# Kernel optimization log

Hardware: AMD Instinct MI355X
Metric: run time of the kernel (lower is better)

The kernel has to match this reference:

```python
import jax, jax.numpy as jnp
import numpy as np

B, S, D = 4, 2048, 1024
NEG = 1e9


def setup_inputs() -> dict:
    key = jax.random.key(0)
    ks = jax.random.split(key, 4)
    scale = 1.0 / np.sqrt(D)  # glorot-ish init scale for stability
    x = jax.random.normal(ks[0], (B, S, D), dtype=jnp.float32)
    Wq = jax.random.normal(ks[1], (D, D), dtype=jnp.float32) * scale
    Wk = jax.random.normal(ks[2], (D, D), dtype=jnp.float32) * scale
    Wv = jax.random.normal(ks[3], (D, D), dtype=jnp.float32) * scale
    bq = jnp.zeros((D,), jnp.float32)
    bk = jnp.zeros((D,), jnp.float32)
    bv = jnp.zeros((D,), jnp.float32)
    return {"x": x, "Wq": Wq, "bq": bq, "Wk": Wk, "bk": bk, "Wv": Wv, "bv": bv}


def reference(x, Wq, bq, Wk, bk, Wv, bv):
    # Dense projections (single head, no 1/sqrt(d) scaling, matching source)
    q = x @ Wq + bq                      # [B,S,D]
    k = x @ Wk + bk                      # [B,S,D]
    v = x @ Wv + bv                      # [B,S,D]
    scores = jnp.einsum('bqd,bkd->bqk', q, k)   # [B,S,S]
    seq = scores.shape[-1]
    mask = jnp.tril(jnp.ones((seq, seq), scores.dtype))  # lower-triangular causal
    scores = scores * mask - NEG * (1.0 - mask)
    weights = jax.nn.softmax(scores, axis=-1)
    return jnp.einsum('bqk,bkd->bqd', weights, v)
```

## Files before the change

kernel.cpp:

```cpp
#include <hip/hip_runtime.h>

typedef float f32x4  __attribute__((ext_vector_type(4)));
typedef _Float16 f16x8  __attribute__((ext_vector_type(8)));
typedef _Float16 f16x4v __attribute__((ext_vector_type(4)));
typedef _Float16 f16x8v __attribute__((ext_vector_type(8)));

__device__ inline void load_lds16(const _Float16* g, _Float16* l) {
    __builtin_amdgcn_global_load_lds((const __attribute__((address_space(1))) void*)g,
                                     (__attribute__((address_space(3))) void*)l, 16, 0, 0);
}

__global__ __launch_bounds__(256)
void convert_h(const float* __restrict__ X, _Float16* __restrict__ H, long n4)
{
    long i = (long)blockIdx.x * 256 + threadIdx.x;
    if (i >= n4) return;
    f32x4 v = ((const f32x4*)X)[i];
    f16x4v h;
#pragma unroll
    for (int k = 0; k < 4; ++k) h[k] = (_Float16)v[k];
    ((f16x4v*)H)[i] = h;
}

__global__ __launch_bounds__(256)
void transpose_w3(const float* __restrict__ Wq, const float* __restrict__ Wk,
                  const float* __restrict__ Wv,
                  _Float16* __restrict__ W2, _Float16* __restrict__ Wvt, int D)
{
    const int z = blockIdx.z;
    const float* W = (z == 0) ? Wq : (z == 1) ? Wk : Wv;

    __shared__ float t[32][33];
    const int tid = threadIdx.x;
    const int bx = blockIdx.x * 32, by = blockIdx.y * 32;
    const int c = tid & 31, r0 = tid >> 5;
#pragma unroll
    for (int r = r0; r < 32; r += 8)
        t[r][c] = W[(long)(by + r) * D + bx + c];
    __syncthreads();
#pragma unroll
    for (int r = r0; r < 32; r += 8) {
        float v = t[c][r];
        _Float16 h = (_Float16)v;
        if (z < 2) {
            const long nrow = (long)z * D + bx + r;
            W2[nrow * 2 * D + by + c]     = h;
            W2[nrow * 2 * D + D + by + c] = (_Float16)(v - (float)h);
        } else {
            Wvt[(long)(bx + r) * D + by + c] = h;
        }
    }
}

__global__ __launch_bounds__(512)
void proj8(const _Float16* __restrict__ x_h, const _Float16* __restrict__ W2,
           const _Float16* __restrict__ Wvt,
           _Float16* __restrict__ Q_h, _Float16* __restrict__ K_h,
           _Float16* __restrict__ K_l, _Float16* __restrict__ Vt,
           const float* __restrict__ bq, const float* __restrict__ bk,
           const float* __restrict__ bv)
{
    constexpr int D = 1024, SEQ = 2048, BK = 64;
    __shared__ __align__(16) _Float16 lds[65536];

    const int orig = blockIdx.x;
    const bool isV = orig >= 256;
    int ct, rt, ldb, NT;
    const _Float16* Bb;
    if (!isV) {
        const int x = orig & 7, i = orig >> 3;
        rt = x * 4 + (i & 3);  ct = i >> 2;
        Bb = W2;  ldb = 2 * D; NT = 32;
    } else {
        const int o = orig - 256, x = o & 7, i = o >> 3;
        rt = x * 4 + (i & 3);  ct = i >> 2;
        Bb = Wvt; ldb = D;     NT = 16;
    }
    const int row0 = rt * 256, col0 = ct * 256;

    const int tid = threadIdx.x;
    const int wave = tid >> 6, lane = tid & 63, l16 = lane & 15, quad = lane >> 4;
    const int wmh = (wave >> 2) * 128;
    const int wn  = (wave & 3) * 64;

    _Float16* SA = lds;
    _Float16* SB = lds + 32768;

#define STAGEH(gb, ld, grow0, gk, dst)                                          \
    {                                                                           \
        _Pragma("unroll")                                                       \
        for (int q_ = 0; q_ < 2; ++q_) {                                        \
            const int p_ = q_ * 512 + tid;                                      \
            const int rw_ = p_ >> 3;                                            \
            const int kq_ = (p_ & 7) ^ (rw_ & 7);                               \
            load_lds16((gb) + (long)((grow0) + rw_) * (ld) + (gk) + kq_ * 8,    \
                       (dst) + p_ * 8);                                         \
        }                                                                       \
    }

    STAGEH(Bb, ldb, col0,       0, SB);
    STAGEH(Bb, ldb, col0 + 128, 0, SB + 8192);
    STAGEH(x_h, D, row0,        0, SA);
    STAGEH(x_h, D, row0 + 128,  0, SA + 8192);
    asm volatile("s_waitcnt vmcnt(0)" ::: "memory");
    __syncthreads();

    f32x4 acc[8][4] = {};

    for (int t = 0; t < NT; ++t) {
        const int cur = t & 1;
        _Float16* Ac = SA + cur * 16384;
        _Float16* Bc = SB + cur * 16384;
        _Float16* An = SA + (cur ^ 1) * 16384;
        _Float16* Bn = SB + (cur ^ 1) * 16384;
        const bool pf = (t + 1 < NT);
        const int kA = ((t + 1) * BK) & (D - 1);
        const int kB = (t + 1) * BK;

        f16x8 b[4][2];
#pragma unroll
        for (int p = 0; p < 4; ++p) {
            if (p == 0) {
#pragma unroll
                for (int j = 0; j < 4; ++j) {
                    const int nr = wn + j * 16 + l16;
#pragma unroll
                    for (int kk = 0; kk < 2; ++kk)
                        b[j][kk] = *(const f16x8*)&Bc[nr * 64 +
                                        ((((kk << 2) | quad) ^ (nr & 7)) << 3)];
                }
            }
            f16x8 a[2][2];
#pragma unroll
            for (int il = 0; il < 2; ++il) {
                const int lr = wmh + (p * 2 + il) * 16 + l16;
#pragma unroll
                for (int kk = 0; kk < 2; ++kk)
                    a[il][kk] = *(const f16x8*)&Ac[lr * 64 +
                                    ((((kk << 2) | quad) ^ (lr & 7)) << 3)];
            }
            if (pf) {
                if (p == 0) { STAGEH(Bb, ldb, col0,       kB, Bn);
                              STAGEH(Bb, ldb, col0 + 128, kB, Bn + 8192); }
                if (p == 1) { STAGEH(x_h, D, row0,        kA, An);
                              STAGEH(x_h, D, row0 + 128,  kA, An + 8192); }
            }
            if (p == 2) asm volatile("s_waitcnt vmcnt(4)" ::: "memory");
            if (p == 3) asm volatile("s_waitcnt vmcnt(0)" ::: "memory");
            __builtin_amdgcn_s_barrier();
            asm volatile("s_waitcnt lgkmcnt(0)" ::: "memory");
            __builtin_amdgcn_sched_barrier(0);
            __builtin_amdgcn_s_setprio(1);
#pragma unroll
            for (int il = 0; il < 2; ++il)
#pragma unroll
                for (int j = 0; j < 4; ++j)
#pragma unroll
                    for (int kk = 0; kk < 2; ++kk)
                        acc[p * 2 + il][j] = __builtin_amdgcn_mfma_f32_16x16x32_f16(
                            a[il][kk], b[j][kk], acc[p * 2 + il][j], 0, 0, 0);
            __builtin_amdgcn_s_setprio(0);
            __builtin_amdgcn_s_barrier();
        }
    }

    if (!isV) {
        const bool isQ = ct < 4;
        const float* bias = isQ ? bq : bk;
#pragma unroll
        for (int j = 0; j < 4; ++j) {
            const int colg = col0 + wn + j * 16 + l16;
            const int cc = isQ ? colg : colg - D;
            const float bval = bias[cc];
#pragma unroll
            for (int i = 0; i < 8; ++i) {
                const int rb = row0 + wmh + i * 16 + quad * 4;
#pragma unroll
                for (int r = 0; r < 4; ++r) {
                    const float v = acc[i][j][r] + bval;
                    const _Float16 h = (_Float16)v;
                    if (isQ) {
                        Q_h[(long)(rb + r) * D + cc] = h;
                    } else {
                        K_h[(long)(rb + r) * D + cc] = h;
                        K_l[(long)(rb + r) * D + cc] = (_Float16)(v - (float)h);
                    }
                }
            }
        }
    } else {
        _Float16* sVt = lds;
#pragma unroll
        for (int j = 0; j < 4; ++j) {
            const int cl = wn + j * 16 + l16;
            const float bval = bv[col0 + cl];
#pragma unroll
            for (int i = 0; i < 8; ++i) {
                f16x4v pk;
#pragma unroll
                for (int r = 0; r < 4; ++r) pk[r] = (_Float16)(acc[i][j][r] + bval);
                const int rowb = wmh * 2 + i * 32 + quad * 8;
                const int sb = cl * 512 + (rowb ^ ((cl & 31) << 4));
                *(f16x4v*)((char*)sVt + sb) = pk;
            }
        }
        __syncthreads();
        const int bb = row0 >> 11;
        const int s0 = row0 & (SEQ - 1);
        for (int idx = tid; idx < 8192; idx += 512) {
            const int cl = idx >> 5, r8 = idx & 31;
            const int sb = cl * 512 + ((r8 * 16) ^ ((cl & 31) << 4));
            f16x8v v = *(const f16x8v*)((char*)sVt + sb);
            *(f16x8v*)&Vt[((long)bb * D + col0 + cl) * SEQ + s0 + r8 * 8] = v;
        }
    }
#undef STAGEH
}

constexpr int TM = 128, TK = 32;

template<bool BLO, int MODE, int TNB>
__global__ __launch_bounds__(256)
void gemm2(const _Float16* __restrict__ Ah, long sA, int lda,
           const _Float16* __restrict__ Bh, const _Float16* __restrict__ Bl,
           long sB, int ldb,
           float* __restrict__ Cf, long sC, int ldc, int K)
{
    static_assert(MODE != 1 || TNB == 64, "packed causal decode assumes TNB=64");
    constexpr int NFJ = TNB / 32;
    constexpr int BRNDS = TNB / 64;

    int rt, ct;
    if (MODE == 1) {
        const int t = blockIdx.x;
        rt = (int)((sqrtf(4.0f * t + 1.0f) - 1.0f) * 0.5f);
        while (rt * (rt + 1) > t) --rt;
        while ((rt + 1) * (rt + 2) <= t) ++rt;
        ct = t - rt * (rt + 1);
    } else {
        rt = (gridDim.x - 1) - blockIdx.x;
        ct = blockIdx.y;
    }
    const int bz = blockIdx.z;

    const _Float16* gAh = Ah + (long)bz * sA;
    const _Float16* gBh = Bh + (long)bz * sB;
    const _Float16* gBl = BLO ? Bl + (long)bz * sB : nullptr;

    const int row0 = rt * TM, col0 = ct * TNB;
    const int k_end = (MODE == 2) ? min(K, (rt + 1) * TM) : K;

    __shared__ _Float16 sAh[TM * TK];
    __shared__ _Float16 sBh[TNB * TK];
    __shared__ _Float16 sBl[BLO ? TNB * TK : 8];

    const int tid = threadIdx.x;
    const int lane = tid & 63, wave = tid >> 6;
    const int l16 = lane & 15, quad = lane >> 4;
    const int wm = (wave >> 1) * 64, wn = (wave & 1) * (TNB / 2);

    f32x4 acc[4][NFJ] = {};

    for (int k0 = 0; k0 < k_end; k0 += TK) {
#pragma unroll
        for (int rnd = 0; rnd < 2; ++rnd) {
            const int row = rnd * 64 + (tid >> 2);
            const long gA = (long)(row0 + row) * lda + k0 + (tid & 3) * 8;
            load_lds16(gAh + gA, sAh + rnd * 2048 + tid * 8);
        }
#pragma unroll
        for (int rnd = 0; rnd < BRNDS; ++rnd) {
            const int row = rnd * 64 + (tid >> 2);
            const long gB = (long)(col0 + row) * ldb + k0 + (tid & 3) * 8;
            const int lofs = rnd * 2048 + tid * 8;
            load_lds16(gBh + gB, sBh + lofs);
            if (BLO) load_lds16(gBl + gB, sBl + lofs);
        }
        __syncthreads();

        f16x8 a[4], b_h[NFJ];
#pragma unroll
        for (int i = 0; i < 4; ++i)
            a[i] = *(const f16x8*)&sAh[(wm + i * 16 + l16) * TK + (quad << 3)];
#pragma unroll
        for (int j = 0; j < NFJ; ++j)
            b_h[j] = *(const f16x8*)&sBh[(wn + j * 16 + l16) * TK + (quad << 3)];

        if (BLO) {
            f16x8 b_l[NFJ];
#pragma unroll
            for (int j = 0; j < NFJ; ++j)
                b_l[j] = *(const f16x8*)&sBl[(wn + j * 16 + l16) * TK + (quad << 3)];
#pragma unroll
            for (int i = 0; i < 4; ++i)
#pragma unroll
                for (int j = 0; j < NFJ; ++j) {
                    acc[i][j] = __builtin_amdgcn_mfma_f32_16x16x32_f16(a[i], b_h[j], acc[i][j], 0, 0, 0);
                    acc[i][j] = __builtin_amdgcn_mfma_f32_16x16x32_f16(a[i], b_l[j], acc[i][j], 0, 0, 0);
                }
        } else {
#pragma unroll
            for (int i = 0; i < 4; ++i)
#pragma unroll
                for (int j = 0; j < NFJ; ++j)
                    acc[i][j] = __builtin_amdgcn_mfma_f32_16x16x32_f16(a[i], b_h[j], acc[i][j], 0, 0, 0);
        }
        __syncthreads();
    }

    float* cf = Cf + (long)bz * sC;
#pragma unroll
    for (int j = 0; j < NFJ; ++j) {
        const int col = col0 + wn + j * 16 + l16;
#pragma unroll
        for (int i = 0; i < 4; ++i) {
            const int rb = row0 + wm + i * 16 + quad * 4;
#pragma unroll
            for (int r = 0; r < 4; ++r)
                cf[(long)(rb + r) * ldc + col] = acc[i][j][r];
        }
    }
}

__global__ __launch_bounds__(256)
void softmax_kernel(const float* __restrict__ Sc, _Float16* __restrict__ P, int seq)
{
    const int r = blockIdx.x, b = blockIdx.y;
    const float* row = Sc + ((long)b * seq + r) * seq;
    _Float16* prow = P + ((long)b * seq + r) * seq;
    const int tid = threadIdx.x;
    const int cmax = ((r >> 7) + 1) << 7;
    const int c0 = tid * 8;

    float v[8];
    f32x4 v0, v1;
    if (c0 <= r) {
        const f32x4* rp = (const f32x4*)row;
        v0 = rp[tid * 2];
        v1 = rp[tid * 2 + 1];
    } else {
        v0 = (f32x4)(-3.0e38f);
        v1 = (f32x4)(-3.0e38f);
    }
    float lmax = -3.0e38f;
#pragma unroll
    for (int k = 0; k < 4; ++k) {
        v[k]     = (c0 + k     <= r) ? v0[k] : -3.0e38f;
        v[k + 4] = (c0 + k + 4 <= r) ? v1[k] : -3.0e38f;
    }
#pragma unroll
    for (int k = 0; k < 8; ++k) lmax = fmaxf(lmax, v[k]);

    __shared__ float red[256];
    red[tid] = lmax; __syncthreads();
    for (int s = 128; s > 0; s >>= 1) {
        if (tid < s) red[tid] = fmaxf(red[tid], red[tid + s]);
        __syncthreads();
    }
    const float m = red[0];
    __syncthreads();

    float lsum = 0.0f;
#pragma unroll
    for (int k = 0; k < 8; ++k) {
        float e = (v[k] > -1.0e38f) ? __expf(v[k] - m) : 0.0f;
        v[k] = e;
        lsum += e;
    }
    red[tid] = lsum; __syncthreads();
    for (int s = 128; s > 0; s >>= 1) {
        if (tid < s) red[tid] += red[tid + s];
        __syncthreads();
    }
    const float inv = 1.0f / red[0];

    if (c0 < cmax) {
        f16x8v o;
#pragma unroll
        for (int k = 0; k < 8; ++k) o[k] = (_Float16)(v[k] * inv);
        ((f16x8v*)prow)[tid] = o;
    }
}

extern "C" void kernel_launch(void* const* d_in, const int* in_sizes, int n_in,
                              void* d_out, int out_size, void* d_ws, size_t ws_size,
                              hipStream_t stream)
{
    constexpr int B = 4, S = 2048, D = 1024;
    constexpr long MB = 1024 * 1024;
    const float* x  = (const float*)d_in[0];
    const float* Wq = (const float*)d_in[1];
    const float* bq = (const float*)d_in[2];
    const float* Wk = (const float*)d_in[3];
    const float* bk = (const float*)d_in[4];
    const float* Wv = (const float*)d_in[5];
    const float* bv = (const float*)d_in[6];
    float* out = (float*)d_out;

    char* ws = (char*)d_ws;
    _Float16* x_h   = (_Float16*)(ws + 0);
    _Float16* W2    = (_Float16*)(ws + 16 * MB);
    _Float16* Wvt_h = (_Float16*)(ws + 24 * MB);
    float*    Sc    = (float*)(ws + 0);
    _Float16* Q_h   = (_Float16*)(ws + 64 * MB);
    _Float16* K_h   = (_Float16*)(ws + 80 * MB);
    _Float16* K_l   = (_Float16*)(ws + 96 * MB);
    _Float16* Vt    = (_Float16*)(ws + 112 * MB);
    _Float16* P     = (_Float16*)(ws + 128 * MB);

    const int M = B * S;
    dim3 blk(256);

    convert_h<<<(M * D / 4 + 255) / 256, blk, 0, stream>>>(x, x_h, (long)M * D / 4);
    transpose_w3<<<dim3(D / 32, D / 32, 3), blk, 0, stream>>>(
        Wq, Wk, Wv, W2, Wvt_h, D);

    proj8<<<dim3(384), dim3(512), 0, stream>>>(
        x_h, W2, Wvt_h, Q_h, K_h, K_l, Vt, bq, bk, bv);

    const int ntiles = (S / TM) * (S / TM + 1);
    gemm2<true, 1, 64><<<dim3(ntiles, 1, B), blk, 0, stream>>>(
        Q_h, (long)S * D, D, K_h, K_l, (long)S * D, D,
        Sc, (long)S * S, S, D);

    softmax_kernel<<<dim3(S, B), blk, 0, stream>>>(Sc, P, S);

    gemm2<false, 2, 64><<<dim3(S / TM, D / 64, B), blk, 0, stream>>>(
        P, (long)S * S, S, Vt, nullptr, (long)D * S, S,
        out, (long)S * D, D, S);
}
```

Baseline: 338.4 us.

## Restructure projection GEMM into four-slot K=32 ring buffer with depth-two prefetch

The projection kernel's main loop moves from double-buffered K=64 tiles to a four-slot ring of K=32 slices, prefetching two slices ahead. Each slice is split into two MFMA phases, and the A and B loads are spread across those phases with finer vmcnt waits. The aim is to hide global-to-LDS latency more deeply and to reduce register pressure from holding fragments. The cost is more barriers per unit of K and a more complex LDS swizzle mapping.

```diff
diff --git a/kernel.cpp b/kernel.cpp
--- a/kernel.cpp
+++ b/kernel.cpp
@@ -60,21 +60,21 @@
            const float* __restrict__ bq, const float* __restrict__ bk,
            const float* __restrict__ bv)
 {
-    constexpr int D = 1024, SEQ = 2048, BK = 64;
+    constexpr int D = 1024, SEQ = 2048;
     __shared__ __align__(16) _Float16 lds[65536];
 
     const int orig = blockIdx.x;
     const bool isV = orig >= 256;
-    int ct, rt, ldb, NT;
+    int ct, rt, ldb, NT2;
     const _Float16* Bb;
     if (!isV) {
         const int x = orig & 7, i = orig >> 3;
         rt = x * 4 + (i & 3);  ct = i >> 2;
-        Bb = W2;  ldb = 2 * D; NT = 32;
+        Bb = W2;  ldb = 2 * D; NT2 = 64;
     } else {
         const int o = orig - 256, x = o & 7, i = o >> 3;
         rt = x * 4 + (i & 3);  ct = i >> 2;
-        Bb = Wvt; ldb = D;     NT = 16;
+        Bb = Wvt; ldb = D;     NT2 = 32;
     }
     const int row0 = rt * 256, col0 = ct * 256;
 
@@ -82,86 +82,88 @@
     const int wave = tid >> 6, lane = tid & 63, l16 = lane & 15, quad = lane >> 4;
     const int wmh = (wave >> 2) * 128;
     const int wn  = (wave & 3) * 64;
-
-    _Float16* SA = lds;
-    _Float16* SB = lds + 32768;
-
-#define STAGEH(gb, ld, grow0, gk, dst)                                          \
+    const int ahalf = (wave >> 2) << 2;
+
+#define STAGES(gb, ld, base0, kbase, dst)                                       \
     {                                                                           \
         _Pragma("unroll")                                                       \
         for (int q_ = 0; q_ < 2; ++q_) {                                        \
             const int p_ = q_ * 512 + tid;                                      \
-            const int rw_ = p_ >> 3;                                            \
-            const int kq_ = (p_ & 7) ^ (rw_ & 7);                               \
-            load_lds16((gb) + (long)((grow0) + rw_) * (ld) + (gk) + kq_ * 8,    \
+            const int rp_ = p_ >> 3;                                            \
+            const int gl_ = (p_ & 7) ^ (rp_ & 7);                               \
+            const int row_ = rp_ + ((gl_ >> 2) << 7);                           \
+            load_lds16((gb) + (long)((base0) + row_) * (ld) + (kbase) +         \
+                           ((gl_ & 3) << 3),                                    \
                        (dst) + p_ * 8);                                         \
         }                                                                       \
     }
 
-    STAGEH(Bb, ldb, col0,       0, SB);
-    STAGEH(Bb, ldb, col0 + 128, 0, SB + 8192);
-    STAGEH(x_h, D, row0,        0, SA);
-    STAGEH(x_h, D, row0 + 128,  0, SA + 8192);
-    asm volatile("s_waitcnt vmcnt(0)" ::: "memory");
+    STAGES(x_h, D, row0, 0,  lds);
+    STAGES(Bb, ldb, col0, 0, lds + 32768);
+    STAGES(x_h, D, row0, 32, lds + 8192);
+    STAGES(Bb, ldb, col0, 32, lds + 32768 + 8192);
+    asm volatile("s_waitcnt vmcnt(4)" ::: "memory");
     __syncthreads();
 
     f32x4 acc[8][4] = {};
 
-    for (int t = 0; t < NT; ++t) {
-        const int cur = t & 1;
-        _Float16* Ac = SA + cur * 16384;
-        _Float16* Bc = SB + cur * 16384;
-        _Float16* An = SA + (cur ^ 1) * 16384;
-        _Float16* Bn = SB + (cur ^ 1) * 16384;
-        const bool pf = (t + 1 < NT);
-        const int kA = ((t + 1) * BK) & (D - 1);
-        const int kB = (t + 1) * BK;
-
-        f16x8 b[4][2];
-#pragma unroll
-        for (int p = 0; p < 4; ++p) {
-            if (p == 0) {
-#pragma unroll
-                for (int j = 0; j < 4; ++j) {
-                    const int nr = wn + j * 16 + l16;
-#pragma unroll
-                    for (int kk = 0; kk < 2; ++kk)
-                        b[j][kk] = *(const f16x8*)&Bc[nr * 64 +
-                                        ((((kk << 2) | quad) ^ (nr & 7)) << 3)];
-                }
-            }
-            f16x8 a[2][2];
-#pragma unroll
-            for (int il = 0; il < 2; ++il) {
-                const int lr = wmh + (p * 2 + il) * 16 + l16;
-#pragma unroll
-                for (int kk = 0; kk < 2; ++kk)
-                    a[il][kk] = *(const f16x8*)&Ac[lr * 64 +
-                                    ((((kk << 2) | quad) ^ (lr & 7)) << 3)];
-            }
-            if (pf) {
-                if (p == 0) { STAGEH(Bb, ldb, col0,       kB, Bn);
-                              STAGEH(Bb, ldb, col0 + 128, kB, Bn + 8192); }
-                if (p == 1) { STAGEH(x_h, D, row0,        kA, An);
-                              STAGEH(x_h, D, row0 + 128,  kA, An + 8192); }
-            }
-            if (p == 2) asm volatile("s_waitcnt vmcnt(4)" ::: "memory");
-            if (p == 3) asm volatile("s_waitcnt vmcnt(0)" ::: "memory");
-            __builtin_amdgcn_s_barrier();
-            asm volatile("s_waitcnt lgkmcnt(0)" ::: "memory");
-            __builtin_amdgcn_sched_barrier(0);
-            __builtin_amdgcn_s_setprio(1);
-#pragma unroll
-            for (int il = 0; il < 2; ++il)
-#pragma unroll
-                for (int j = 0; j < 4; ++j)
-#pragma unroll
-                    for (int kk = 0; kk < 2; ++kk)
-                        acc[p * 2 + il][j] = __builtin_amdgcn_mfma_f32_16x16x32_f16(
-                            a[il][kk], b[j][kk], acc[p * 2 + il][j], 0, 0, 0);
-            __builtin_amdgcn_s_setprio(0);
-            __builtin_amdgcn_s_barrier();
-        }
+    for (int s = 0; s < NT2; ++s) {
+        _Float16* Asl = lds + (s & 3) * 8192;
+        _Float16* Bsl = lds + 32768 + (s & 3) * 8192;
+        const bool pf = (s + 2 < NT2);
+        const int kA2 = ((s + 2) * 32) & (D - 1);
+        const int kB2 = (s + 2) * 32;
+
+        f16x8 b[4], a0[4];
+#pragma unroll
+        for (int j = 0; j < 4; ++j) {
+            const int nr = wn + j * 16 + l16;
+            const int rpb = nr & 127;
+            const int gpb = ((((nr >> 7) << 2) | quad) ^ (rpb & 7));
+            b[j] = *(const f16x8*)&Bsl[rpb * 64 + gpb * 8];
+        }
+#pragma unroll
+        for (int il = 0; il < 4; ++il) {
+            const int rp = il * 16 + l16;
+            const int gpa = ((ahalf | quad) ^ (rp & 7));
+            a0[il] = *(const f16x8*)&Asl[rp * 64 + gpa * 8];
+        }
+        if (pf) STAGES(x_h, D, row0, kA2, lds + ((s + 2) & 3) * 8192);
+        __builtin_amdgcn_s_barrier();
+        asm volatile("s_waitcnt lgkmcnt(0)" ::: "memory");
+        __builtin_amdgcn_sched_barrier(0);
+        __builtin_amdgcn_s_setprio(1);
+#pragma unroll
+        for (int il = 0; il < 4; ++il)
+#pragma unroll
+            for (int j = 0; j < 4; ++j)
+                acc[il][j] = __builtin_amdgcn_mfma_f32_16x16x32_f16(
+                    a0[il], b[j], acc[il][j], 0, 0, 0);
+        __builtin_amdgcn_s_setprio(0);
+        __builtin_amdgcn_s_barrier();
+
+        f16x8 a1[4];
+#pragma unroll
+        for (int il = 0; il < 4; ++il) {
+            const int rp = (il + 4) * 16 + l16;
+            const int gpa = ((ahalf | quad) ^ (rp & 7));
+            a1[il] = *(const f16x8*)&Asl[rp * 64 + gpa * 8];
+        }
+        if (pf) STAGES(Bb, ldb, col0, kB2, lds + 32768 + ((s + 2) & 3) * 8192);
+        if (pf)                asm volatile("s_waitcnt vmcnt(4)" ::: "memory");
+        else if (s + 1 < NT2)  asm volatile("s_waitcnt vmcnt(0)" ::: "memory");
+        __builtin_amdgcn_s_barrier();
+        asm volatile("s_waitcnt lgkmcnt(0)" ::: "memory");
+        __builtin_amdgcn_sched_barrier(0);
+        __builtin_amdgcn_s_setprio(1);
+#pragma unroll
+        for (int il = 0; il < 4; ++il)
+#pragma unroll
+            for (int j = 0; j < 4; ++j)
+                acc[4 + il][j] = __builtin_amdgcn_mfma_f32_16x16x32_f16(
+                    a1[il], b[j], acc[4 + il][j], 0, 0, 0);
+        __builtin_amdgcn_s_setprio(0);
+        __builtin_amdgcn_s_barrier();
     }
 
     if (!isV) {
@@ -210,11 +212,11 @@
         for (int idx = tid; idx < 8192; idx += 512) {
             const int cl = idx >> 5, r8 = idx & 31;
             const int sb = cl * 512 + ((r8 * 16) ^ ((cl & 31) << 4));
-            f16x8v v = *(const f16x8v*)((char*)sVt + sb);
+            f16x8v v = *(const f16x8v*)&((char*)sVt)[sb];
             *(f16x8v*)&Vt[((long)bb * D + col0 + cl) * SEQ + s0 + r8 * 8] = v;
         }
     }
-#undef STAGEH
+#undef STAGES
 }
 
 constexpr int TM = 128, TK = 32;
```

Result: no change. 341.9 us (+1.0%).
